# Performance work log

Measured on AMD Instinct MI355X. Metric: run time of the kernel, lower is better.

Reference implementation:

```python
import jax, jax.numpy as jnp
import numpy as np

L, P, D, AL = 48, 2048, 50, 5
ONEHOT = 5 * D + 5  # 255, leaf one-hot size per encode()


def setup_inputs() -> dict:
    rng = np.random.default_rng(0)
    # node types: 0=leaf 1=unary 2=exist 3=univ 4=binary 5=functor 6=predicate
    node_type = np.zeros((L, P), np.int64)
    node_type[1:] = rng.integers(0, 7, size=(L - 1, P))
    children = -np.ones((L, P, AL), np.int64)
    for l in range(1, L):
        hi = l * P  # children must come from earlier levels (topological order)
        nt = node_type[l]
        n_child = np.where(nt == 0, 0,
                  np.where(nt <= 3, 1,
                  np.where(nt == 4, 2, rng.integers(1, AL + 1, size=P))))
        samp = rng.integers(0, hi, size=(P, AL))
        m = np.arange(AL)[None, :] < n_child[:, None]
        children[l] = np.where(m, samp, -1)
    # two-hot leaf encoding per encode(): v[category]=1 (0..4) and v[i+5]=1
    cat = rng.integers(0, 5, size=(L, P))
    ident = rng.integers(0, 5 * D, size=(L, P))
    onehot = np.zeros((L, P, ONEHOT), np.float32)
    li, pi = np.meshgrid(np.arange(L), np.arange(P), indexing='ij')
    onehot[li, pi, ident + 5] = 1.0
    onehot[li, pi, cat] = 1.0

    def lin(i, out_d, in_d):
        k = jax.random.fold_in(jax.random.key(0), i)
        kw, kb = jax.random.split(k)
        W = jax.random.normal(kw, (out_d, in_d), jnp.float32) * (in_d ** -0.5)
        b = jax.random.normal(kb, (out_d,), jnp.float32) * 0.01
        return W, b

    W_leaf, b_leaf = lin(0, D, ONEHOT)
    W_unary, b_unary = lin(1, D, D)
    W_exist, b_exist = lin(2, D, D)
    W_univ, b_univ = lin(3, D, D)
    W_bin, b_bin = lin(4, D, 3 * D)
    W_fun, b_fun = lin(5, D, (1 + AL) * D)
    W_pred, b_pred = lin(6, D, (1 + AL) * D)
    W_final, b_final = lin(7, ONEHOT, D)
    return dict(node_type=jnp.asarray(node_type, jnp.int32),
                children=jnp.asarray(children, jnp.int32),
                onehot=jnp.asarray(onehot),
                W_leaf=W_leaf, b_leaf=b_leaf, W_unary=W_unary, b_unary=b_unary,
                W_exist=W_exist, b_exist=b_exist, W_univ=W_univ, b_univ=b_univ,
                W_bin=W_bin, b_bin=b_bin, W_fun=W_fun, b_fun=b_fun,
                W_pred=W_pred, b_pred=b_pred, W_final=W_final, b_final=b_final)


def reference(node_type, children, onehot,
              W_leaf, b_leaf, W_unary, b_unary, W_exist, b_exist,
              W_univ, b_univ, W_bin, b_bin, W_fun, b_fun,
              W_pred, b_pred, W_final, b_final):
    relu = jax.nn.relu

    def step(buf, xs):
        l, nt, ch, oh = xs  # nt:[P], ch:[P,AL], oh:[P,ONEHOT]
        leaf = relu(oh @ W_leaf.T + b_leaf)                      # relu(leaf_net(onehot))
        mask = (ch >= 0).astype(buf.dtype)[..., None]
        ce = buf[jnp.clip(ch, 0)] * mask                          # [P,AL,D] child embeddings
        c0, c1 = ce[:, 0], ce[:, 1]
        unary = relu(c0 @ W_unary.T + b_unary)
        exist = relu(c0 @ W_exist.T + b_exist)
        univ = relu(c0 @ W_univ.T + b_univ)
        binv = relu(jnp.concatenate([c0, leaf, c1], -1) @ W_bin.T + b_bin)  # cat[left, op, right]
        fin = jnp.concatenate([leaf, ce.reshape(P, AL * D)], -1)  # [P,(1+AL)*D]
        fun = relu(fin @ W_fun.T + b_fun)
        pred = relu(fin @ W_pred.T + b_pred)
        outs = jnp.stack([leaf, unary, exist, univ, binv, fun, pred])  # [7,P,D]
        out = jnp.take_along_axis(outs, nt[None, :, None], axis=0)[0]
        buf = jax.lax.dynamic_update_slice(buf, out, (l * P, 0))
        return buf, None

    buf0 = jnp.zeros((L * P, D), onehot.dtype)
    xs = (jnp.arange(L), node_type, children, onehot)
    buf, _ = jax.lax.scan(step, buf0, xs)
    root = buf[-1]
    return root @ W_final.T + b_final  # self.final(self.visit(input)), shape [255]
```

## Files before the change

### kernel.cpp

```cpp
#include <hip/hip_runtime.h>

#define L_ 48
#define P_ 2048
#define D_ 50
#define AL_ 5
#define OH_ 255
#define NNODES (L_*P_)
#define MAXN_ 256
#define HSZ 512
#define NTHREADS 512
#define NWAVES 8
#define GRID_ 256
#define SPIN_BOUND (1 << 22)

__device__ __forceinline__ float dot50L(const float* __restrict__ Wg, const float* inL) {
    const float4* x4 = (const float4*)inL;
    float a0 = 0.f, a1 = 0.f, a2 = 0.f, a3 = 0.f;
    #pragma unroll
    for (int q = 0; q < 12; ++q) {
        float4 x = x4[q];
        float2 w0 = *(const float2*)(Wg + q * 4);
        float2 w1 = *(const float2*)(Wg + q * 4 + 2);
        a0 += w0.x * x.x; a1 += w0.y * x.y;
        a2 += w1.x * x.z; a3 += w1.y * x.w;
    }
    float4 xt = x4[12];
    float2 wt = *(const float2*)(Wg + 48);
    a0 += wt.x * xt.x; a1 += wt.y * xt.y;
    return (a0 + a1) + (a2 + a3);
}

__device__ __forceinline__ float dot50LL(const float* WL, const float* xL) {
    const float4* w4 = (const float4*)WL;
    const float4* x4 = (const float4*)xL;
    float a0 = 0.f, a1 = 0.f, a2 = 0.f, a3 = 0.f;
    #pragma unroll
    for (int q = 0; q < 12; ++q) {
        float4 w = w4[q], x = x4[q];
        a0 += w.x * x.x; a1 += w.y * x.y;
        a2 += w.z * x.z; a3 += w.w * x.w;
    }
    float2 wt = *(const float2*)(WL + 48);
    float2 xt = *(const float2*)(xL + 48);
    a0 += wt.x * xt.x; a1 += wt.y * xt.y;
    return (a0 + a1) + (a2 + a3);
}

__device__ __forceinline__ float dotrow(const float* __restrict__ W, const float* in, int len) {
    float a0 = 0.f, a1 = 0.f, a2 = 0.f, a3 = 0.f;
    int j = 0;
    for (; j + 4 <= len; j += 4) {
        a0 += W[j] * in[j]; a1 += W[j+1] * in[j+1];
        a2 += W[j+2] * in[j+2]; a3 += W[j+3] * in[j+3];
    }
    for (; j < len; ++j) a0 += W[j] * in[j];
    return (a0 + a1) + (a2 + a3);
}

__device__ __forceinline__ float pf4(const float* __restrict__ p, int n, int t, int nth) {
    float s = 0.f;
    for (int i = t * 4; i + 3 < n; i += nth * 4) {
        float4 v = *reinterpret_cast<const float4*>(p + i);
        s += v.x + v.y + v.z + v.w;
    }
    return s;
}

__global__ __launch_bounds__(NTHREADS)
void formula_kernel(const int* __restrict__ node_type,
                    const int* __restrict__ children,
                    const float* __restrict__ onehot,
                    const float* __restrict__ W_leaf,  const float* __restrict__ b_leaf,
                    const float* __restrict__ W_unary, const float* __restrict__ b_unary,
                    const float* __restrict__ W_exist, const float* __restrict__ b_exist,
                    const float* __restrict__ W_univ,  const float* __restrict__ b_univ,
                    const float* __restrict__ W_bin,   const float* __restrict__ b_bin,
                    const float* __restrict__ W_fun,   const float* __restrict__ b_fun,
                    const float* __restrict__ W_pred,  const float* __restrict__ b_pred,
                    const float* __restrict__ W_final, const float* __restrict__ b_final,
                    float* __restrict__ out)
{
    if (blockIdx.x != 0) {
        const int t   = (int)threadIdx.x + ((int)blockIdx.x - 1) * NTHREADS;
        const int nth = (GRID_ - 1) * NTHREADS;
        int is = 0;
        const int4* c4 = (const int4*)children;
        for (int i = t; i < (NNODES * AL_) / 4; i += nth) { int4 v = c4[i]; is += v.x + v.y + v.z + v.w; }
        const int4* n4 = (const int4*)node_type;
        for (int i = t; i < NNODES / 4; i += nth) { int4 v = n4[i]; is += v.x + v.y + v.z + v.w; }
        float s = 0.f;
        s += pf4(W_leaf,  D_ * OH_,    t, nth);
        s += pf4(W_unary, D_ * D_,     t, nth);
        s += pf4(W_exist, D_ * D_,     t, nth);
        s += pf4(W_univ,  D_ * D_,     t, nth);
        s += pf4(W_bin,   D_ * 3 * D_, t, nth);
        s += pf4(W_fun,   D_ * 6 * D_, t, nth);
        s += pf4(W_pred,  D_ * 6 * D_, t, nth);
        s += pf4(W_final, OH_ * D_,    t, nth);
        if (t < 64) {
            int j = t % D_;
            s += b_leaf[j] + b_unary[j] + b_exist[j] + b_univ[j]
               + b_bin[j] + b_fun[j] + b_pred[j] + b_final[t % OH_];
        }
        asm volatile("" :: "v"(s), "v"(is));
        return;
    }

    __shared__ int h_key[HSZ];
    __shared__ int h_val[HSZ];
    __shared__ int list[MAXN_];
    __shared__ int nt_l[MAXN_];
    __shared__ int order[MAXN_];
    __shared__ int rdy[MAXN_];
    __shared__ int ch_l[MAXN_][AL_];
    __shared__ int cnt_sh, done_sh;
    __shared__ __align__(16) float emb_s[MAXN_][52];
    __shared__ __align__(16) float leaf_s[MAXN_][52];
    __shared__ __align__(16) float W_lds[3][D_][52];
    __shared__ int   nzj[NWAVES][16];
    __shared__ float nzv[NWAVES][16];

    const int tid  = threadIdx.x;
    const int lane = tid & 63;
    const int wave = tid >> 6;

    h_key[tid & (HSZ - 1)] = -1;
    if (tid == 0) { cnt_sh = 1; done_sh = 0; list[0] = NNODES - 1; }
    __syncthreads();

    if (wave == 0) {
        if (lane == 0) {
            const int root = NNODES - 1;
            unsigned h = ((unsigned)root * 2654435761u) >> 16;
            for (;;) { int i = (int)(h & (HSZ - 1));
                       if (h_key[i] == -1) { h_key[i] = root; h_val[i] = 0; break; } ++h; }
        }
        __builtin_amdgcn_wave_barrier();

        int total_reg = 1;
        int fs = 0, fe = 1;
        while (fs < fe) {
            int ic = 0;
            for (int i = fs + lane; i < fe; i += 64) {
                int n = list[i];
                int cv[AL_];
                #pragma unroll
                for (int k = 0; k < AL_; ++k) cv[k] = children[(size_t)n * AL_ + k];
                #pragma unroll
                for (int k = 0; k < AL_; ++k) ch_l[i][k] = cv[k];
                #pragma unroll
                for (int k = 0; k < AL_; ++k) {
                    int c = cv[k];
                    if (c >= 0) {
                        unsigned h = ((unsigned)c * 2654435761u) >> 16;
                        for (;;) {
                            int s2 = (int)(h & (HSZ - 1));
                            int prev = atomicCAS(&h_key[s2], -1, c);
                            if (prev == -1) {
                                int pos = atomicAdd(&cnt_sh, 1);
                                h_val[s2] = pos;
                                if (pos < MAXN_) list[pos] = c;
                                ic++;
                                break;
                            }
                            if (prev == c) break;
                            ++h;
                        }
                    }
                }
            }
            __builtin_amdgcn_wave_barrier();
            int tot = ic;
            #pragma unroll
            for (int d = 1; d < 64; d <<= 1) tot += __shfl_xor(tot, d);
            total_reg += tot;
            fs = fe;
            fe = (total_reg < MAXN_) ? total_reg : MAXN_;
            __builtin_amdgcn_wave_barrier();
        }
        if (lane == 0) *((volatile int*)&done_sh) = 1;
    } else if (wave == 1) {
        float s = 0.f;
        if (lane < D_) s += b_leaf[lane] + b_unary[lane] + b_exist[lane] + b_univ[lane]
                          + b_bin[lane] + b_fun[lane] + b_pred[lane];
        for (int j = lane; j < OH_; j += 64) s += b_final[j];
        volatile int* vc = &cnt_sh;
        volatile int* vd = &done_sh;
        int seen = 0;
        for (;;) {
            int done = *vd;
            int c = *vc;
            if (c > MAXN_) c = MAXN_;
            for (int i = seen; i < c; ++i) {
                int n = list[i];
                if ((unsigned)n >= (unsigned)NNODES) n = 0;
                const float* oh = onehot + (size_t)n * OH_;
                if (lane < 63) {
                    int j = lane * 4;
                    s += oh[j] + oh[j+1] + oh[j+2] + oh[j+3];
                } else {
                    s += (float)node_type[n];
                    s += (float)(children[(size_t)n * AL_] + children[(size_t)n * AL_ + 4]);
                }
            }
            seen = c;
            if (done) break;
        }
        asm volatile("" :: "v"(s));
    } else {
        const int t = tid - 128, nth = NTHREADS - 128;
        for (int e = t; e < 3 * D_ * D_; e += nth) {
            int m = e / (D_ * D_), r = e % (D_ * D_);
            const float* Wm = (m == 0) ? W_unary : (m == 1) ? W_exist : W_univ;
            W_lds[m][r / D_][r % D_] = Wm[r];
        }
        float s = 0.f;
        s += pf4(W_leaf,  D_ * OH_,    t, nth);
        s += pf4(W_bin,   D_ * 3 * D_, t, nth);
        s += pf4(W_fun,   D_ * 6 * D_, t, nth);
        s += pf4(W_pred,  D_ * 6 * D_, t, nth);
        s += pf4(W_final, OH_ * D_,    t, nth);
        asm volatile("" :: "v"(s));
    }
    __syncthreads();

    const int count = (cnt_sh < MAXN_) ? cnt_sh : MAXN_;

    for (int t = tid; t < count * AL_; t += NTHREADS) {
        int i = t / AL_, k = t % AL_;
        int c = ch_l[i][k];
        if (c >= 0) {
            int sl = -1;
            unsigned h = ((unsigned)c * 2654435761u) >> 16;
            for (;;) {
                int ii = (int)(h & (HSZ - 1));
                if (h_key[ii] == c) { sl = h_val[ii]; break; }
                ++h;
            }
            if (sl >= MAXN_) sl = -1;
            ch_l[i][k] = sl;
        }
    }
    for (int i = tid; i < count; i += NTHREADS) {
        int me = list[i];
        nt_l[i] = node_type[me];
        int r = 0;
        for (int j = 0; j < count; ++j) r += (list[j] < me);
        order[r] = i;
        rdy[i] = 0;
    }
    __syncthreads();

    for (int slot = wave; slot < count; slot += NWAVES) {
        const int nt = nt_l[slot];
        if (nt >= 1 && nt <= 3) continue;
        const int n = list[slot];
        const float* oh = onehot + (size_t)n * OH_;
        float v[4]; int c2 = 0;
        #pragma unroll
        for (int t = 0; t < 4; ++t) {
            int j = lane * 4 + t;
            v[t] = (j < OH_) ? oh[j] : 0.0f;
            if (v[t] != 0.0f) c2++;
        }
        int incl = c2;
        #pragma unroll
        for (int dlt = 1; dlt < 64; dlt <<= 1) {
            int o = __shfl_up(incl, dlt);
            if (lane >= dlt) incl += o;
        }
        const int excl = incl - c2;
        const int total = __shfl(incl, 63);
        if (total <= 16) {
            int p2 = excl;
            #pragma unroll
            for (int t = 0; t < 4; ++t)
                if (v[t] != 0.0f) { nzj[wave][p2] = lane * 4 + t; nzv[wave][p2] = v[t]; p2++; }
        }
        __builtin_amdgcn_wave_barrier();
        if (lane < D_) {
            float sacc = b_leaf[lane];
            if (total <= 16) {
                for (int i2 = 0; i2 < total; ++i2)
                    sacc += nzv[wave][i2] * W_leaf[lane * OH_ + nzj[wave][i2]];
            } else {
                sacc += dotrow(W_leaf + lane * OH_, oh, OH_);
            }
            float lv = fmaxf(sacc, 0.0f);
            if (nt == 0) { emb_s[slot][lane] = lv; }
            else         { leaf_s[slot][lane] = lv; }
        }
        if (nt == 0 && lane == 0) rdy[slot] = 1;
        __builtin_amdgcn_wave_barrier();
    }
    __syncthreads();

    volatile int* vrdy = rdy;
    for (int pos = wave; pos < count; pos += NWAVES) {
        const int slot = order[pos];
        const int nt = nt_l[slot];
        if (nt == 0) continue;

        #pragma unroll
        for (int k = 0; k < AL_; ++k) {
            int cs = ch_l[slot][k];
            if (cs >= 0) {
                int guard = 0;
                while (vrdy[cs] == 0 && guard < SPIN_BOUND) ++guard;
            }
        }
        __threadfence_block();

        float outv = 0.0f;
        if (lane < D_) {
            float s;
            if (nt <= 3) {
                const float* b = (nt == 1) ? b_unary : (nt == 2) ? b_exist : b_univ;
                s = b[lane];
                const int cs0 = ch_l[slot][0];
                if (cs0 >= 0) s += dot50LL(W_lds[nt - 1][lane], emb_s[cs0]);
            } else if (nt == 4) {
                const float* W = W_bin + lane * 3 * D_;
                s = b_bin[lane];
                const int cs0 = ch_l[slot][0], cs1 = ch_l[slot][1];
                if (cs0 >= 0) s += dot50L(W, emb_s[cs0]);
                s += dot50L(W + D_, leaf_s[slot]);
                if (cs1 >= 0) s += dot50L(W + 2 * D_, emb_s[cs1]);
            } else {
                const float* W = ((nt == 5) ? W_fun : W_pred) + lane * 6 * D_;
                s = ((nt == 5) ? b_fun : b_pred)[lane] + dot50L(W, leaf_s[slot]);
                #pragma unroll
                for (int k = 0; k < AL_; ++k) {
                    int cs = ch_l[slot][k];
                    if (cs >= 0) s += dot50L(W + (1 + k) * D_, emb_s[cs]);
                }
            }
            outv = fmaxf(s, 0.0f);
        }
        if (lane < D_) emb_s[slot][lane] = outv;
        __threadfence_block();
        if (lane == 0) vrdy[slot] = 1;
    }
    __syncthreads();

    const int rootslot = order[count - 1];
    for (int o = tid; o < OH_; o += NTHREADS)
        out[o] = b_final[o] + dot50L(W_final + o * D_, emb_s[rootslot]);
}

extern "C" void kernel_launch(void* const* d_in, const int* in_sizes, int n_in,
                              void* d_out, int out_size, void* d_ws, size_t ws_size,
                              hipStream_t stream) {
    const int*   node_type = (const int*)d_in[0];
    const int*   children  = (const int*)d_in[1];
    const float* onehot    = (const float*)d_in[2];
    const float* W_leaf  = (const float*)d_in[3];  const float* b_leaf  = (const float*)d_in[4];
    const float* W_unary = (const float*)d_in[5];  const float* b_unary = (const float*)d_in[6];
    const float* W_exist = (const float*)d_in[7];  const float* b_exist = (const float*)d_in[8];
    const float* W_univ  = (const float*)d_in[9];  const float* b_univ  = (const float*)d_in[10];
    const float* W_bin   = (const float*)d_in[11]; const float* b_bin   = (const float*)d_in[12];
    const float* W_fun   = (const float*)d_in[13]; const float* b_fun   = (const float*)d_in[14];
    const float* W_pred  = (const float*)d_in[15]; const float* b_pred  = (const float*)d_in[16];
    const float* W_final = (const float*)d_in[17]; const float* b_final = (const float*)d_in[18];

    float* out = (float*)d_out;

    formula_kernel<<<GRID_, NTHREADS, 0, stream>>>(
        node_type, children, onehot,
        W_leaf, b_leaf, W_unary, b_unary, W_exist, b_exist, W_univ, b_univ,
        W_bin, b_bin, W_fun, b_fun, W_pred, b_pred, W_final, b_final,
        out);
}
```

Measured before the change: 24.24 us.

## Overlap leaf embedding with dependency discovery and prefetch weight rows into registers

Waves other than the discovery wave now pull newly discovered nodes from a shared counter and compute their node type and leaf embeddings while the BFS is still running, replacing the former warm-up-only loops and the separate leaf pass after sorting. The leaf embedding is stored directly in emb_s, and the separate leaf_s buffer is removed. For binary, functor and predicate nodes, the first 96 weights are loaded into registers before waiting on the children, and the concatenated input is staged in a per-wave LDS buffer so a single contiguous dot product can run. Biases move to LDS, the discovery wave gets raised priority, and the children/node_type prefetch in the helper blocks is dropped. The costs are more register pressure, spin-wait polling between waves, and a dependence on correct ordering between the producer and consumer waves.

```diff
diff --git a/kernel.cpp b/kernel.cpp
--- a/kernel.cpp
+++ b/kernel.cpp
@@ -66,7 +66,7 @@
     return s;
 }
 
-__global__ __launch_bounds__(NTHREADS)
+__global__ __launch_bounds__(NTHREADS, 2)
 void formula_kernel(const int* __restrict__ node_type,
                     const int* __restrict__ children,
                     const float* __restrict__ onehot,
@@ -83,11 +83,6 @@
     if (blockIdx.x != 0) {
         const int t   = (int)threadIdx.x + ((int)blockIdx.x - 1) * NTHREADS;
         const int nth = (GRID_ - 1) * NTHREADS;
-        int is = 0;
-        const int4* c4 = (const int4*)children;
-        for (int i = t; i < (NNODES * AL_) / 4; i += nth) { int4 v = c4[i]; is += v.x + v.y + v.z + v.w; }
-        const int4* n4 = (const int4*)node_type;
-        for (int i = t; i < NNODES / 4; i += nth) { int4 v = n4[i]; is += v.x + v.y + v.z + v.w; }
         float s = 0.f;
         s += pf4(W_leaf,  D_ * OH_,    t, nth);
         s += pf4(W_unary, D_ * D_,     t, nth);
@@ -102,7 +97,7 @@
             s += b_leaf[j] + b_unary[j] + b_exist[j] + b_univ[j]
                + b_bin[j] + b_fun[j] + b_pred[j] + b_final[t % OH_];
         }
-        asm volatile("" :: "v"(s), "v"(is));
+        asm volatile("" :: "v"(s));
         return;
     }
 
@@ -113,10 +108,11 @@
     __shared__ int order[MAXN_];
     __shared__ int rdy[MAXN_];
     __shared__ int ch_l[MAXN_][AL_];
-    __shared__ int cnt_sh, done_sh;
+    __shared__ int cnt_sh, done_sh, next_sh;
     __shared__ __align__(16) float emb_s[MAXN_][52];
-    __shared__ __align__(16) float leaf_s[MAXN_][52];
     __shared__ __align__(16) float W_lds[3][D_][52];
+    __shared__ __align__(16) float b_lds[6][52];
+    __shared__ __align__(16) float xbuf[NWAVES][304];
     __shared__ int   nzj[NWAVES][16];
     __shared__ float nzv[NWAVES][16];
 
@@ -124,11 +120,20 @@
     const int lane = tid & 63;
     const int wave = tid >> 6;
 
-    h_key[tid & (HSZ - 1)] = -1;
-    if (tid == 0) { cnt_sh = 1; done_sh = 0; list[0] = NNODES - 1; }
+    h_key[tid] = -1;
+    if (tid > 0 && tid < MAXN_) { list[tid] = -1; rdy[tid] = 0; }
+    if (tid == 0) {
+        cnt_sh = 1; done_sh = 0; next_sh = 0;
+        list[0] = NNODES - 1; rdy[0] = 0;
+    }
     __syncthreads();
 
+    volatile int* vc = &cnt_sh;
+    volatile int* vd = &done_sh;
+    volatile int* vlist = list;
+
     if (wave == 0) {
+        __builtin_amdgcn_s_setprio(1);
         if (lane == 0) {
             const int root = NNODES - 1;
             unsigned h = ((unsigned)root * 2654435761u) >> 16;
@@ -141,31 +146,26 @@
         int fs = 0, fe = 1;
         while (fs < fe) {
             int ic = 0;
-            for (int i = fs + lane; i < fe; i += 64) {
-                int n = list[i];
-                int cv[AL_];
-                #pragma unroll
-                for (int k = 0; k < AL_; ++k) cv[k] = children[(size_t)n * AL_ + k];
-                #pragma unroll
-                for (int k = 0; k < AL_; ++k) ch_l[i][k] = cv[k];
-                #pragma unroll
-                for (int k = 0; k < AL_; ++k) {
-                    int c = cv[k];
-                    if (c >= 0) {
-                        unsigned h = ((unsigned)c * 2654435761u) >> 16;
-                        for (;;) {
-                            int s2 = (int)(h & (HSZ - 1));
-                            int prev = atomicCAS(&h_key[s2], -1, c);
-                            if (prev == -1) {
-                                int pos = atomicAdd(&cnt_sh, 1);
-                                h_val[s2] = pos;
-                                if (pos < MAXN_) list[pos] = c;
-                                ic++;
-                                break;
-                            }
-                            if (prev == c) break;
-                            ++h;
+            const int pairs = (fe - fs) * AL_;
+            for (int t = lane; t < pairs; t += 64) {
+                const int i = fs + t / AL_;
+                const int k = t - (t / AL_) * AL_;
+                const int c = children[(size_t)list[i] * AL_ + k];
+                ch_l[i][k] = c;
+                if (c >= 0) {
+                    unsigned h = ((unsigned)c * 2654435761u) >> 16;
+                    for (;;) {
+                        int s2 = (int)(h & (HSZ - 1));
+                        int prev = atomicCAS(&h_key[s2], -1, c);
+                        if (prev == -1) {
+                            int pos = atomicAdd(&cnt_sh, 1);
+                            h_val[s2] = pos;
+                            if (pos < MAXN_) list[pos] = c;
+                            ic++;
+                            break;
                         }
+                        if (prev == c) break;
+                        ++h;
                     }
                 }
             }
@@ -178,49 +178,76 @@
             fe = (total_reg < MAXN_) ? total_reg : MAXN_;
             __builtin_amdgcn_wave_barrier();
         }
-        if (lane == 0) *((volatile int*)&done_sh) = 1;
-    } else if (wave == 1) {
-        float s = 0.f;
-        if (lane < D_) s += b_leaf[lane] + b_unary[lane] + b_exist[lane] + b_univ[lane]
-                          + b_bin[lane] + b_fun[lane] + b_pred[lane];
-        for (int j = lane; j < OH_; j += 64) s += b_final[j];
-        volatile int* vc = &cnt_sh;
-        volatile int* vd = &done_sh;
-        int seen = 0;
+        __builtin_amdgcn_s_setprio(0);
+        if (lane == 0) *vd = 1;
+    } else {
+        if (wave >= 1 && wave <= 3) {
+            const int m = wave - 1;
+            const float* Wm = (m == 0) ? W_unary : (m == 1) ? W_exist : W_univ;
+            for (int j = lane; j < D_ * D_; j += 64)
+                W_lds[m][j / D_][j % D_] = Wm[j];
+        } else if (wave == 4) {
+            if (lane < D_) {
+                b_lds[0][lane] = b_unary[lane]; b_lds[1][lane] = b_exist[lane];
+                b_lds[2][lane] = b_univ[lane];  b_lds[3][lane] = b_bin[lane];
+                b_lds[4][lane] = b_fun[lane];   b_lds[5][lane] = b_pred[lane];
+            }
+        }
         for (;;) {
-            int done = *vd;
-            int c = *vc;
-            if (c > MAXN_) c = MAXN_;
-            for (int i = seen; i < c; ++i) {
-                int n = list[i];
-                if ((unsigned)n >= (unsigned)NNODES) n = 0;
+            int i0 = 0;
+            if (lane == 0) i0 = atomicAdd(&next_sh, 1);
+            i0 = __shfl(i0, 0);
+            bool ok = false;
+            for (;;) {
+                int c = *vc; if (c > MAXN_) c = MAXN_;
+                if (i0 < c) { ok = true; break; }
+                if (*vd) break;
+                __builtin_amdgcn_s_sleep(1);
+            }
+            if (!ok) break;
+            int n;
+            while ((n = vlist[i0]) < 0) {}
+            if ((unsigned)n >= (unsigned)NNODES) n = 0;
+            const int nt = node_type[n];
+            if (lane == 0) nt_l[i0] = nt;
+            if (nt == 0 || nt >= 4) {
                 const float* oh = onehot + (size_t)n * OH_;
-                if (lane < 63) {
-                    int j = lane * 4;
-                    s += oh[j] + oh[j+1] + oh[j+2] + oh[j+3];
-                } else {
-                    s += (float)node_type[n];
-                    s += (float)(children[(size_t)n * AL_] + children[(size_t)n * AL_ + 4]);
-                }
-            }
-            seen = c;
-            if (done) break;
-        }
-        asm volatile("" :: "v"(s));
-    } else {
-        const int t = tid - 128, nth = NTHREADS - 128;
-        for (int e = t; e < 3 * D_ * D_; e += nth) {
-            int m = e / (D_ * D_), r = e % (D_ * D_);
-            const float* Wm = (m == 0) ? W_unary : (m == 1) ? W_exist : W_univ;
-            W_lds[m][r / D_][r % D_] = Wm[r];
-        }
-        float s = 0.f;
-        s += pf4(W_leaf,  D_ * OH_,    t, nth);
-        s += pf4(W_bin,   D_ * 3 * D_, t, nth);
-        s += pf4(W_fun,   D_ * 6 * D_, t, nth);
-        s += pf4(W_pred,  D_ * 6 * D_, t, nth);
-        s += pf4(W_final, OH_ * D_,    t, nth);
-        asm volatile("" :: "v"(s));
+                float v[4]; int c2 = 0;
+                #pragma unroll
+                for (int t = 0; t < 4; ++t) {
+                    int j = lane * 4 + t;
+                    v[t] = (j < OH_) ? oh[j] : 0.0f;
+                    if (v[t] != 0.0f) c2++;
+                }
+                int incl = c2;
+                #pragma unroll
+                for (int dlt = 1; dlt < 64; dlt <<= 1) {
+                    int o = __shfl_up(incl, dlt);
+                    if (lane >= dlt) incl += o;
+                }
+                const int excl = incl - c2;
+                const int total = __shfl(incl, 63);
+                if (total <= 16) {
+                    int p2 = excl;
+                    #pragma unroll
+                    for (int t = 0; t < 4; ++t)
+                        if (v[t] != 0.0f) { nzj[wave][p2] = lane * 4 + t; nzv[wave][p2] = v[t]; p2++; }
+                }
+                __builtin_amdgcn_wave_barrier();
+                if (lane < D_) {
+                    float sacc = b_leaf[lane];
+                    if (total <= 16) {
+                        for (int i2 = 0; i2 < total; ++i2)
+                            sacc += nzv[wave][i2] * W_leaf[lane * OH_ + nzj[wave][i2]];
+                    } else {
+                        sacc += dotrow(W_leaf + lane * OH_, oh, OH_);
+                    }
+                    emb_s[i0][lane] = fmaxf(sacc, 0.0f);
+                }
+                __builtin_amdgcn_wave_barrier();
+                if (nt == 0 && lane == 0) rdy[i0] = 1;
+            }
+        }
     }
     __syncthreads();
 
@@ -243,55 +270,9 @@
     }
     for (int i = tid; i < count; i += NTHREADS) {
         int me = list[i];
-        nt_l[i] = node_type[me];
         int r = 0;
         for (int j = 0; j < count; ++j) r += (list[j] < me);
         order[r] = i;
-        rdy[i] = 0;
-    }
-    __syncthreads();
-
-    for (int slot = wave; slot < count; slot += NWAVES) {
-        const int nt = nt_l[slot];
-        if (nt >= 1 && nt <= 3) continue;
-        const int n = list[slot];
-        const float* oh = onehot + (size_t)n * OH_;
-        float v[4]; int c2 = 0;
-        #pragma unroll
-        for (int t = 0; t < 4; ++t) {
-            int j = lane * 4 + t;
-            v[t] = (j < OH_) ? oh[j] : 0.0f;
-            if (v[t] != 0.0f) c2++;
-        }
-        int incl = c2;
-        #pragma unroll
-        for (int dlt = 1; dlt < 64; dlt <<= 1) {
-            int o = __shfl_up(incl, dlt);
-            if (lane >= dlt) incl += o;
-        }
-        const int excl = incl - c2;
-        const int total = __shfl(incl, 63);
-        if (total <= 16) {
-            int p2 = excl;
-            #pragma unroll
-            for (int t = 0; t < 4; ++t)
-                if (v[t] != 0.0f) { nzj[wave][p2] = lane * 4 + t; nzv[wave][p2] = v[t]; p2++; }
-        }
-        __builtin_amdgcn_wave_barrier();
-        if (lane < D_) {
-            float sacc = b_leaf[lane];
-            if (total <= 16) {
-                for (int i2 = 0; i2 < total; ++i2)
-                    sacc += nzv[wave][i2] * W_leaf[lane * OH_ + nzj[wave][i2]];
-            } else {
-                sacc += dotrow(W_leaf + lane * OH_, oh, OH_);
-            }
-            float lv = fmaxf(sacc, 0.0f);
-            if (nt == 0) { emb_s[slot][lane] = lv; }
-            else         { leaf_s[slot][lane] = lv; }
-        }
-        if (nt == 0 && lane == 0) rdy[slot] = 1;
-        __builtin_amdgcn_wave_barrier();
     }
     __syncthreads();
 
@@ -301,41 +282,82 @@
         const int nt = nt_l[slot];
         if (nt == 0) continue;
 
-        #pragma unroll
-        for (int k = 0; k < AL_; ++k) {
-            int cs = ch_l[slot][k];
-            if (cs >= 0) {
-                int guard = 0;
-                while (vrdy[cs] == 0 && guard < SPIN_BOUND) ++guard;
-            }
-        }
-        __threadfence_block();
-
         float outv = 0.0f;
-        if (lane < D_) {
-            float s;
-            if (nt <= 3) {
-                const float* b = (nt == 1) ? b_unary : (nt == 2) ? b_exist : b_univ;
-                s = b[lane];
-                const int cs0 = ch_l[slot][0];
+        if (nt <= 3) {
+            const int cs0 = ch_l[slot][0];
+            if (cs0 >= 0) {
+                int g = 0;
+                while (vrdy[cs0] == 0 && g < SPIN_BOUND) ++g;
+            }
+            __threadfence_block();
+            if (lane < D_) {
+                float s = b_lds[nt - 1][lane];
                 if (cs0 >= 0) s += dot50LL(W_lds[nt - 1][lane], emb_s[cs0]);
-            } else if (nt == 4) {
-                const float* W = W_bin + lane * 3 * D_;
-                s = b_bin[lane];
-                const int cs0 = ch_l[slot][0], cs1 = ch_l[slot][1];
-                if (cs0 >= 0) s += dot50L(W, emb_s[cs0]);
-                s += dot50L(W + D_, leaf_s[slot]);
-                if (cs1 >= 0) s += dot50L(W + 2 * D_, emb_s[cs1]);
-            } else {
-                const float* W = ((nt == 5) ? W_fun : W_pred) + lane * 6 * D_;
-                s = ((nt == 5) ? b_fun : b_pred)[lane] + dot50L(W, leaf_s[slot]);
+                outv = fmaxf(s, 0.0f);
+            }
+        } else {
+            const int len = (nt == 4) ? 150 : 300;
+            const float* Wrow = (nt == 4) ? (W_bin + lane * 150)
+                              : (nt == 5) ? (W_fun + lane * 300)
+                                          : (W_pred + lane * 300);
+            float4 wreg[24];
+            if (lane < D_) {
                 #pragma unroll
-                for (int k = 0; k < AL_; ++k) {
-                    int cs = ch_l[slot][k];
-                    if (cs >= 0) s += dot50L(W + (1 + k) * D_, emb_s[cs]);
-                }
-            }
-            outv = fmaxf(s, 0.0f);
+                for (int q = 0; q < 24; ++q)
+                    wreg[q] = *reinterpret_cast<const float4*>(Wrow + 4 * q);
+            }
+            #pragma unroll
+            for (int k = 0; k < AL_; ++k) {
+                const int cs = ch_l[slot][k];
+                if (cs >= 0) {
+                    int g = 0;
+                    while (vrdy[cs] == 0 && g < SPIN_BOUND) ++g;
+                }
+            }
+            __threadfence_block();
+            for (int j = lane; j < len; j += 64) {
+                const int seg = j / 50, col = j - seg * 50;
+                float v;
+                if (nt == 4) {
+                    if (seg == 0) { int cc = ch_l[slot][0]; v = (cc >= 0) ? emb_s[cc][col] : 0.f; }
+                    else if (seg == 1) v = emb_s[slot][col];
+                    else { int cc = ch_l[slot][1]; v = (cc >= 0) ? emb_s[cc][col] : 0.f; }
+                } else {
+                    if (seg == 0) v = emb_s[slot][col];
+                    else { int cc = ch_l[slot][seg - 1]; v = (cc >= 0) ? emb_s[cc][col] : 0.f; }
+                }
+                xbuf[wave][j] = v;
+            }
+            if (lane < 4) xbuf[wave][len + lane] = 0.f;
+            __builtin_amdgcn_wave_barrier();
+            if (lane < D_) {
+                float s = (nt == 4) ? b_lds[3][lane] : (nt == 5) ? b_lds[4][lane] : b_lds[5][lane];
+                const float4* x4 = (const float4*)xbuf[wave];
+                float a0 = 0.f, a1 = 0.f, a2 = 0.f, a3 = 0.f;
+                #pragma unroll
+                for (int q = 0; q < 24; ++q) {
+                    float4 w = wreg[q], x = x4[q];
+                    a0 += w.x * x.x; a1 += w.y * x.y; a2 += w.z * x.z; a3 += w.w * x.w;
+                }
+                if (nt == 4) {
+                    #pragma unroll
+                    for (int q = 24; q < 37; ++q) {
+                        float4 w = *(const float4*)(Wrow + 4 * q); float4 x = x4[q];
+                        a0 += w.x * x.x; a1 += w.y * x.y; a2 += w.z * x.z; a3 += w.w * x.w;
+                    }
+                    float2 w2 = *(const float2*)(Wrow + 148);
+                    a0 += w2.x * xbuf[wave][148];
+                    a1 += w2.y * xbuf[wave][149];
+                } else {
+                    #pragma unroll
+                    for (int q = 24; q < 75; ++q) {
+                        float4 w = *(const float4*)(Wrow + 4 * q); float4 x = x4[q];
+                        a0 += w.x * x.x; a1 += w.y * x.y; a2 += w.z * x.z; a3 += w.w * x.w;
+                    }
+                }
+                s += (a0 + a1) + (a2 + a3);
+                outv = fmaxf(s, 0.0f);
+            }
         }
         if (lane < D_) emb_s[slot][lane] = outv;
         __threadfence_block();
```

Result: faster. 23.05 us (median of 2 runs) (-4.9%).
